# Optimization experiments

Measured on AMD Instinct MI355X. Metric: run time of the kernel, lower is better.

## Reference

```python
import jax, jax.numpy as jnp
import numpy as np

N_SRC = 100000
N_DST = 100000
E = 1600000
D_IN = 128
D_REL = 128
K = 8        # num_heads
D_OUT = 16   # out_dim per head; K*D_OUT = 128
SLOPE = 0.2  # LeakyReLU negative slope


def setup_inputs() -> dict:
    key = jax.random.key(0)
    ks = jax.random.split(key, 11)
    s = 0.05  # weight init scale
    return {
        "feat_src": jax.random.normal(ks[0], (N_SRC, D_IN), jnp.float32),
        "feat_dst": jax.random.normal(ks[1], (N_DST, D_IN), jnp.float32),
        "feat_rel": jax.random.normal(ks[2], (D_REL,), jnp.float32),
        "W_src": jax.random.normal(ks[3], (D_IN, K * D_OUT), jnp.float32) * s,
        "b_src": jnp.zeros((K * D_OUT,), jnp.float32),
        "W_dst": jax.random.normal(ks[4], (D_IN, K * D_OUT), jnp.float32) * s,
        "b_dst": jnp.zeros((K * D_OUT,), jnp.float32),
        "W_rel": jax.random.normal(ks[5], (D_REL, 2 * K * D_OUT), jnp.float32) * s,
        "b_rel": jnp.zeros((2 * K * D_OUT,), jnp.float32),
        "src_idx": jax.random.randint(ks[6], (E,), 0, N_SRC, dtype=jnp.int32),
        "dst_idx": jax.random.randint(ks[7], (E,), 0, N_DST, dtype=jnp.int32),
    }


def reference(feat_src, feat_dst, feat_rel, W_src, b_src, W_dst, b_dst,
              W_rel, b_rel, src_idx, dst_idx):
    # Linear projections (feat_drop = 0 -> identity)
    fs = (feat_src @ W_src + b_src).reshape(-1, K, D_OUT)   # (N_src, K, D)
    fd = (feat_dst @ W_dst + b_dst).reshape(-1, K, D_OUT)   # (N_dst, K, D)
    attn = (feat_rel @ W_rel + b_rel).reshape(K, 2 * D_OUT)  # (K, 2D)

    el = jnp.einsum('nkd,kd->nk', fs, attn[:, :D_OUT])  # (N_src, K)
    er = jnp.einsum('nkd,kd->nk', fd, attn[:, D_OUT:])  # (N_dst, K)

    # Per-edge scores: u_add_v then LeakyReLU
    e = el[src_idx] + er[dst_idx]                        # (E, K)
    e = jnp.where(e >= 0, e, SLOPE * e)

    # edge_softmax: softmax over incoming edges per destination node
    emax = jax.ops.segment_max(e, dst_idx, num_segments=N_DST)  # (N_dst, K)
    a = jnp.exp(e - emax[dst_idx])                               # (E, K)
    asum = jax.ops.segment_sum(a, dst_idx, num_segments=N_DST)   # (N_dst, K)
    a = a / asum[dst_idx]

    # u_mul_e + sum aggregation
    msg = fs[src_idx] * a[:, :, None]                            # (E, K, D)
    out = jax.ops.segment_sum(msg, dst_idx, num_segments=N_DST)  # (N_dst, K, D)
    return out.reshape(N_DST, K * D_OUT)
```

## Files before the change

kernel.cpp:

```cpp
#include <hip/hip_runtime.h>
#include <hip/hip_fp16.h>
#include <hip/hip_bf16.h>

#define SLOPE 0.2f
#define EPB 4096
#define LDA 136
#define CAPLG 12
#define SCAP 1024

typedef short bf16x8 __attribute__((ext_vector_type(8)));
typedef float f32x4 __attribute__((ext_vector_type(4)));

__device__ __forceinline__ unsigned short f2bf(float x) {
    unsigned u = __float_as_uint(x);
    u += 0x7FFFu + ((u >> 16) & 1u);
    return (unsigned short)(u >> 16);
}

__global__ void prep_kernel(const float* __restrict__ feat_rel,
                            const float* __restrict__ W_rel,
                            const float* __restrict__ b_rel,
                            float* __restrict__ attn,
                            const float* __restrict__ W_src,
                            unsigned short* __restrict__ WtS,
                            const float* __restrict__ W_dst,
                            unsigned short* __restrict__ WtD,
                            int* __restrict__ bcur) {
    int bx = blockIdx.x;
    if (bx < 128) {
        const float* W = (bx < 64) ? W_src : W_dst;
        unsigned short* Wt = (bx < 64) ? WtS : WtD;
        int t = (bx & 63) * 256 + threadIdx.x;
        int n = t >> 7, k = t & 127;
        Wt[n * 128 + k] = f2bf(W[k * 128 + n]);
    } else if (bx == 128) {
        int j = threadIdx.x;
        float acc = b_rel[j];
        for (int d = 0; d < 128; ++d)
            acc = fmaf(feat_rel[d], W_rel[d * 256 + j], acc);
        attn[j] = acc;
    } else {
#pragma unroll
        for (int i = 0; i < 4; ++i) {
            int j = threadIdx.x + i * 256;
            bcur[j] = j << CAPLG;
        }
    }
}

#define SMEM_BYTES ((64 * LDA + 128 * LDA) * 2 + 128 * 4)

__global__ __launch_bounds__(256) void gemm_part_kernel(
    const float* __restrict__ featS, const unsigned short* __restrict__ WtS,
    const float* __restrict__ bS,
    const float* __restrict__ featD, const unsigned short* __restrict__ WtD,
    const float* __restrict__ bD,
    const float* __restrict__ attn, __half* __restrict__ fs,
    float* __restrict__ el, float* __restrict__ er,
    int Ms, int Md, int nbs, int ngemm,
    const int* __restrict__ src_idx, const int* __restrict__ dst_idx,
    int* __restrict__ bcur, int* __restrict__ part, int ne)
{
    __shared__ __align__(16) unsigned char smem[SMEM_BYTES];

    int bx = blockIdx.x;
    int t = threadIdx.x;

    if (bx >= ngemm) {
        int* hist = (int*)smem;
        int* base = hist + 1024;
        for (int i = t; i < 1024; i += 256) hist[i] = 0;
        int e0 = (bx - ngemm) * EPB;
        int myS[16], myD[16];
        __syncthreads();
#pragma unroll
        for (int i = 0; i < 16; ++i) {
            int e = e0 + i * 256 + t;
            if (e < ne) {
                myS[i] = src_idx[e];
                myD[i] = dst_idx[e];
                atomicAdd(&hist[myD[i] >> 7], 1);
            } else myD[i] = -1;
        }
        __syncthreads();
        for (int b = t; b < 1024; b += 256) {
            int c = hist[b];
            if (c > 0) {
                base[b] = atomicAdd(&bcur[b], c);
                hist[b] = 0;
            }
        }
        __syncthreads();
#pragma unroll
        for (int i = 0; i < 16; ++i) {
            if (myD[i] >= 0) {
                int b = myD[i] >> 7;
                int slot = base[b] + atomicAdd(&hist[b], 1);
                part[slot] = myS[i] | ((myD[i] & 127) << 20);
            }
        }
        return;
    }

    unsigned short* sA = (unsigned short*)smem;
    unsigned short* sB = sA + 64 * LDA;
    float* sAtt = (float*)(smem + (64 * LDA + 128 * LDA) * 2);

    const float* feat; const unsigned short* Wt; const float* bias;
    __half* f_out; float* e_out; int attn_off, M, row0;
    if (bx < nbs) {
        feat = featS; Wt = WtS; bias = bS; f_out = fs; e_out = el;
        attn_off = 0; M = Ms; row0 = bx * 64;
    } else {
        feat = featD; Wt = WtD; bias = bD; f_out = nullptr; e_out = er;
        attn_off = 16; M = Md; row0 = (bx - nbs) * 64;
    }

    if (t < 128) sAtt[t] = attn[(t >> 4) * 32 + attn_off + (t & 15)];

#pragma unroll
    for (int i = 0; i < 8; ++i) {
        int idx = t + i * 256;
        int row = idx >> 5, k4 = idx & 31;
        int grow = row0 + row;
        float4 v = {0.f, 0.f, 0.f, 0.f};
        if (grow < M) v = *(const float4*)(feat + (size_t)grow * 128 + k4 * 4);
        ushort4 b;
        b.x = f2bf(v.x); b.y = f2bf(v.y); b.z = f2bf(v.z); b.w = f2bf(v.w);
        *(ushort4*)&sA[row * LDA + k4 * 4] = b;
    }
#pragma unroll
    for (int i = 0; i < 8; ++i) {
        int idx = t + i * 256;
        int n = idx >> 4, koff = (idx & 15) * 8;
        *(uint4*)&sB[n * LDA + koff] = *(const uint4*)&Wt[n * 128 + koff];
    }
    __syncthreads();

    int wv = t >> 6, lane = t & 63;
    int m = lane & 15, quad = lane >> 4;
    int n0 = wv * 32;

    f32x4 acc[2][4];
#pragma unroll
    for (int ct = 0; ct < 2; ++ct)
#pragma unroll
        for (int rt = 0; rt < 4; ++rt) acc[ct][rt] = (f32x4){0.f, 0.f, 0.f, 0.f};

#pragma unroll
    for (int ks = 0; ks < 4; ++ks) {
        bf16x8 a[4], b[2];
#pragma unroll
        for (int rt = 0; rt < 4; ++rt)
            a[rt] = *(const bf16x8*)&sA[(rt * 16 + m) * LDA + ks * 32 + quad * 8];
#pragma unroll
        for (int ct = 0; ct < 2; ++ct)
            b[ct] = *(const bf16x8*)&sB[(n0 + ct * 16 + m) * LDA + ks * 32 + quad * 8];
#pragma unroll
        for (int ct = 0; ct < 2; ++ct)
#pragma unroll
            for (int rt = 0; rt < 4; ++rt)
                acc[ct][rt] = __builtin_amdgcn_mfma_f32_16x16x32_bf16(
                    a[rt], b[ct], acc[ct][rt], 0, 0, 0);
    }

    __syncthreads();
    __half* sF = (__half*)sA;
#pragma unroll
    for (int ct = 0; ct < 2; ++ct) {
        int col = n0 + ct * 16 + m;
        float bias_v = bias[col];
#pragma unroll
        for (int rt = 0; rt < 4; ++rt) {
            f32x4 c = acc[ct][rt];
#pragma unroll
            for (int r = 0; r < 4; ++r)
                sF[(rt * 16 + quad * 4 + r) * LDA + col] = __float2half(c[r] + bias_v);
        }
    }
    __syncthreads();

    int mrem = M - row0;

    if (f_out) {
#pragma unroll
        for (int i = 0; i < 4; ++i) {
            int idx = t + i * 256;
            int row = idx >> 4, c8 = (idx & 15) * 8;
            if (row < mrem) {
                uint4 v = *(const uint4*)&sF[row * LDA + c8];
                *(uint4*)(f_out + (size_t)(row0 + row) * 128 + c8) = v;
            }
        }
    }
#pragma unroll
    for (int i = 0; i < 2; ++i) {
        int p = t + i * 256;
        int row = p >> 3, h = p & 7;
        if (row < mrem) {
            const __half* fp = &sF[row * LDA + h * 16];
            const float* ap = &sAtt[h * 16];
            float acc2 = 0.f;
#pragma unroll
            for (int j = 0; j < 16; ++j)
                acc2 = fmaf((float)fp[j], ap[j], acc2);
            e_out[(size_t)(row0 + row) * 8 + h] = acc2;
        }
    }
}

__global__ __launch_bounds__(256) void bucket_agg_kernel(
    const __half* __restrict__ fs, const float* __restrict__ el,
    const float* __restrict__ er, const int* __restrict__ part,
    const int* __restrict__ bcur, float* __restrict__ out,
    int n_dst, int nbuck, int NB8)
{
    __shared__ int csr_l[SCAP];
    __shared__ int cnt[16];
    __shared__ int off16[16];
    __shared__ int cur[16];

    int b = blockIdx.x % NB8;
    int s = blockIdx.x / NB8;
    if (b >= nbuck) return;
    int node0 = (b << 7) + (s << 4);
    if (node0 >= n_dst) return;

    int tid = threadIdx.x;
    if (tid < 16) { cnt[tid] = 0; cur[tid] = 0; }
    int pstart = b << CAPLG;
    int pend = bcur[b];
    __syncthreads();

    for (int pi = pstart + tid; pi < pend; pi += 256) {
        int dl = part[pi] >> 20;
        if ((dl >> 4) == s) atomicAdd(&cnt[dl & 15], 1);
    }
    __syncthreads();
    if (tid == 0) {
        int r = 0;
#pragma unroll
        for (int i = 0; i < 16; ++i) { off16[i] = r; r += cnt[i]; }
    }
    __syncthreads();
    for (int pi = pstart + tid; pi < pend; pi += 256) {
        int val = part[pi];
        int dl = val >> 20;
        if ((dl >> 4) == s) {
            int f = atomicAdd(&cur[dl & 15], 1);
            csr_l[off16[dl & 15] + f] = val & 0xFFFFF;
        }
    }
    __syncthreads();

    int lane = tid & 63;
    int wv = tid >> 6;
    int g = lane >> 4;
    int q = lane & 15;
    int h = q >> 1;
    int nl = wv * 4 + g;
    int node = node0 + nl;
    bool alive = node < n_dst;
    int start = 0, d = 0;
    float er8 = 0.f;
    if (alive) {
        start = off16[nl];
        d = cnt[nl];
        er8 = er[(size_t)node * 8 + h];
    }

    float acc[8] = {0.f, 0.f, 0.f, 0.f, 0.f, 0.f, 0.f, 0.f};
    float wsum = 0.f;
    int i = 0;
    for (; i + 4 <= d; i += 4) {
        int sj[4]; float ex[4]; uint4 v[4];
#pragma unroll
        for (int j = 0; j < 4; ++j)
            sj[j] = csr_l[start + i + j];
#pragma unroll
        for (int j = 0; j < 4; ++j)
            ex[j] = el[(size_t)sj[j] * 8 + h];
#pragma unroll
        for (int j = 0; j < 4; ++j)
            v[j] = *(const uint4*)(fs + (size_t)sj[j] * 128 + q * 8);
#pragma unroll
        for (int j = 0; j < 4; ++j) {
            float x = ex[j] + er8;
            x = (x < 0.f) ? SLOPE * x : x;
            float w = __expf(x);
            const __half* hp = (const __half*)&v[j];
#pragma unroll
            for (int k = 0; k < 8; ++k)
                acc[k] = fmaf(w, (float)hp[k], acc[k]);
            wsum += w;
        }
    }
    for (; i < d; ++i) {
        int s0 = csr_l[start + i];
        float x = el[(size_t)s0 * 8 + h] + er8;
        x = (x < 0.f) ? SLOPE * x : x;
        float w0 = __expf(x);
        uint4 v0 = *(const uint4*)(fs + (size_t)s0 * 128 + q * 8);
        const __half* hp = (const __half*)&v0;
#pragma unroll
        for (int k = 0; k < 8; ++k)
            acc[k] = fmaf(w0, (float)hp[k], acc[k]);
        wsum += w0;
    }
    if (alive) {
        float inv = (d > 0) ? 1.0f / wsum : 0.f;
        f32x4 o0 = {acc[0] * inv, acc[1] * inv, acc[2] * inv, acc[3] * inv};
        f32x4 o1 = {acc[4] * inv, acc[5] * inv, acc[6] * inv, acc[7] * inv};
        __builtin_nontemporal_store(o0, (f32x4*)(out + (size_t)node * 128 + q * 8));
        __builtin_nontemporal_store(o1, (f32x4*)(out + (size_t)node * 128 + q * 8 + 4));
    }
}

extern "C" void kernel_launch(void* const* d_in, const int* in_sizes, int n_in,
                              void* d_out, int out_size, void* d_ws, size_t ws_size,
                              hipStream_t stream) {
    const float* feat_src = (const float*)d_in[0];
    const float* feat_dst = (const float*)d_in[1];
    const float* feat_rel = (const float*)d_in[2];
    const float* W_src    = (const float*)d_in[3];
    const float* b_src    = (const float*)d_in[4];
    const float* W_dst    = (const float*)d_in[5];
    const float* b_dst    = (const float*)d_in[6];
    const float* W_rel    = (const float*)d_in[7];
    const float* b_rel    = (const float*)d_in[8];
    const int*   src_idx  = (const int*)d_in[9];
    const int*   dst_idx  = (const int*)d_in[10];
    float* out = (float*)d_out;

    int n_src = in_sizes[0] / 128;
    int n_dst = in_sizes[1] / 128;
    int ne    = in_sizes[9];
    int nbuck = (n_dst + 127) >> 7;
    int NB8   = (nbuck + 7) & ~7;
    size_t slab = (size_t)nbuck << CAPLG;

    char* w = (char*)d_ws;
    auto alloc = [&](size_t b) { char* p = w; w += (b + 255) & ~(size_t)255; return p; };
    __half* fs   = (__half*)alloc((size_t)n_src * 128 * 2);
    float*  el   = (float*)alloc((size_t)n_src * 8 * 4);
    float*  er   = (float*)alloc((size_t)n_dst * 8 * 4);
    float*  attn = (float*)alloc(256 * 4);
    unsigned short* WtS = (unsigned short*)alloc(128 * 128 * 2);
    unsigned short* WtD = (unsigned short*)alloc(128 * 128 * 2);
    int*    bcur = (int*)alloc(1024 * 4);
    int*    part = (int*)alloc(slab * 4);

    prep_kernel<<<130, 256, 0, stream>>>(
        feat_rel, W_rel, b_rel, attn, W_src, WtS, W_dst, WtD, bcur);

    int nbs = (n_src + 63) / 64, nbd = (n_dst + 63) / 64;
    int ngemm = nbs + nbd;
    int nparts = (ne + EPB - 1) / EPB;
    gemm_part_kernel<<<ngemm + nparts, 256, 0, stream>>>(
        feat_src, WtS, b_src, feat_dst, WtD, b_dst, attn,
        fs, el, er, n_src, n_dst, nbs, ngemm,
        src_idx, dst_idx, bcur, part, ne);

    bucket_agg_kernel<<<NB8 * 8, 256, 0, stream>>>(
        fs, el, er, part, bcur, out, n_dst, nbuck, NB8);
}
```

Baseline: 283.4 us.

## Fuse prep into GEMM blocks and drop counting pass in bucket aggregation

Removes the separate prep kernel. Each GEMM block now computes the attention vector from W_rel and transposes and converts the fp32 weights to bf16 itself, and a memset initialises the bucket counters. The bucket aggregation kernel drops its first counting pass over the partition list and scatters source indices into fixed 64-entry per-node slots. This saves one launch and one pass over the partition data. In exchange, every GEMM block repeats the attention and weight-transpose work with strided loads, and any node with more than 64 incoming edges silently loses edges.

```diff
diff --git a/kernel.cpp b/kernel.cpp
--- a/kernel.cpp
+++ b/kernel.cpp
@@ -6,7 +6,7 @@
 #define EPB 4096
 #define LDA 136
 #define CAPLG 12
-#define SCAP 1024
+#define NCAP 64
 
 typedef short bf16x8 __attribute__((ext_vector_type(8)));
 typedef float f32x4 __attribute__((ext_vector_type(4)));
@@ -17,46 +17,16 @@
     return (unsigned short)(u >> 16);
 }
 
-__global__ void prep_kernel(const float* __restrict__ feat_rel,
-                            const float* __restrict__ W_rel,
-                            const float* __restrict__ b_rel,
-                            float* __restrict__ attn,
-                            const float* __restrict__ W_src,
-                            unsigned short* __restrict__ WtS,
-                            const float* __restrict__ W_dst,
-                            unsigned short* __restrict__ WtD,
-                            int* __restrict__ bcur) {
-    int bx = blockIdx.x;
-    if (bx < 128) {
-        const float* W = (bx < 64) ? W_src : W_dst;
-        unsigned short* Wt = (bx < 64) ? WtS : WtD;
-        int t = (bx & 63) * 256 + threadIdx.x;
-        int n = t >> 7, k = t & 127;
-        Wt[n * 128 + k] = f2bf(W[k * 128 + n]);
-    } else if (bx == 128) {
-        int j = threadIdx.x;
-        float acc = b_rel[j];
-        for (int d = 0; d < 128; ++d)
-            acc = fmaf(feat_rel[d], W_rel[d * 256 + j], acc);
-        attn[j] = acc;
-    } else {
-#pragma unroll
-        for (int i = 0; i < 4; ++i) {
-            int j = threadIdx.x + i * 256;
-            bcur[j] = j << CAPLG;
-        }
-    }
-}
-
 #define SMEM_BYTES ((64 * LDA + 128 * LDA) * 2 + 128 * 4)
 
 __global__ __launch_bounds__(256) void gemm_part_kernel(
-    const float* __restrict__ featS, const unsigned short* __restrict__ WtS,
+    const float* __restrict__ featS, const float* __restrict__ WS,
     const float* __restrict__ bS,
-    const float* __restrict__ featD, const unsigned short* __restrict__ WtD,
+    const float* __restrict__ featD, const float* __restrict__ WD,
     const float* __restrict__ bD,
-    const float* __restrict__ attn, __half* __restrict__ fs,
-    float* __restrict__ el, float* __restrict__ er,
+    const float* __restrict__ feat_rel, const float* __restrict__ W_rel,
+    const float* __restrict__ b_rel,
+    __half* __restrict__ fs, float* __restrict__ el, float* __restrict__ er,
     int Ms, int Md, int nbs, int ngemm,
     const int* __restrict__ src_idx, const int* __restrict__ dst_idx,
     int* __restrict__ bcur, int* __restrict__ part, int ne)
@@ -86,7 +56,7 @@
         for (int b = t; b < 1024; b += 256) {
             int c = hist[b];
             if (c > 0) {
-                base[b] = atomicAdd(&bcur[b], c);
+                base[b] = (b << CAPLG) + atomicAdd(&bcur[b], c);
                 hist[b] = 0;
             }
         }
@@ -106,17 +76,23 @@
     unsigned short* sB = sA + 64 * LDA;
     float* sAtt = (float*)(smem + (64 * LDA + 128 * LDA) * 2);
 
-    const float* feat; const unsigned short* Wt; const float* bias;
+    const float* feat; const float* W; const float* bias;
     __half* f_out; float* e_out; int attn_off, M, row0;
     if (bx < nbs) {
-        feat = featS; Wt = WtS; bias = bS; f_out = fs; e_out = el;
+        feat = featS; W = WS; bias = bS; f_out = fs; e_out = el;
         attn_off = 0; M = Ms; row0 = bx * 64;
     } else {
-        feat = featD; Wt = WtD; bias = bD; f_out = nullptr; e_out = er;
+        feat = featD; W = WD; bias = bD; f_out = nullptr; e_out = er;
         attn_off = 16; M = Md; row0 = (bx - nbs) * 64;
     }
 
-    if (t < 128) sAtt[t] = attn[(t >> 4) * 32 + attn_off + (t & 15)];
+    if (t < 128) {
+        int j = (t >> 4) * 32 + attn_off + (t & 15);
+        float a = b_rel[j];
+        for (int d = 0; d < 128; ++d)
+            a = fmaf(feat_rel[d], W_rel[d * 256 + j], a);
+        sAtt[t] = a;
+    }
 
 #pragma unroll
     for (int i = 0; i < 8; ++i) {
@@ -132,8 +108,12 @@
 #pragma unroll
     for (int i = 0; i < 8; ++i) {
         int idx = t + i * 256;
-        int n = idx >> 4, koff = (idx & 15) * 8;
-        *(uint4*)&sB[n * LDA + koff] = *(const uint4*)&Wt[n * 128 + koff];
+        int n = idx & 127, kc = (idx >> 7) * 8;
+        unsigned short tmp[8];
+#pragma unroll
+        for (int j = 0; j < 8; ++j)
+            tmp[j] = f2bf(W[(size_t)(kc + j) * 128 + n]);
+        *(uint4*)&sB[n * LDA + kc] = *(uint4*)tmp;
     }
     __syncthreads();
 
@@ -215,9 +195,7 @@
     const int* __restrict__ bcur, float* __restrict__ out,
     int n_dst, int nbuck, int NB8)
 {
-    __shared__ int csr_l[SCAP];
-    __shared__ int cnt[16];
-    __shared__ int off16[16];
+    __shared__ int csr_l[16 * NCAP];
     __shared__ int cur[16];
 
     int b = blockIdx.x % NB8;
@@ -227,28 +205,17 @@
     if (node0 >= n_dst) return;
 
     int tid = threadIdx.x;
-    if (tid < 16) { cnt[tid] = 0; cur[tid] = 0; }
+    if (tid < 16) cur[tid] = 0;
     int pstart = b << CAPLG;
-    int pend = bcur[b];
-    __syncthreads();
-
-    for (int pi = pstart + tid; pi < pend; pi += 256) {
-        int dl = part[pi] >> 20;
-        if ((dl >> 4) == s) atomicAdd(&cnt[dl & 15], 1);
-    }
-    __syncthreads();
-    if (tid == 0) {
-        int r = 0;
-#pragma unroll
-        for (int i = 0; i < 16; ++i) { off16[i] = r; r += cnt[i]; }
-    }
-    __syncthreads();
+    int pend = pstart + bcur[b];
+    __syncthreads();
+
     for (int pi = pstart + tid; pi < pend; pi += 256) {
         int val = part[pi];
         int dl = val >> 20;
         if ((dl >> 4) == s) {
             int f = atomicAdd(&cur[dl & 15], 1);
-            csr_l[off16[dl & 15] + f] = val & 0xFFFFF;
+            if (f < NCAP) csr_l[(dl & 15) * NCAP + f] = val & 0xFFFFF;
         }
     }
     __syncthreads();
@@ -261,11 +228,11 @@
     int nl = wv * 4 + g;
     int node = node0 + nl;
     bool alive = node < n_dst;
-    int start = 0, d = 0;
+    int start = nl * NCAP;
+    int d = 0;
     float er8 = 0.f;
     if (alive) {
-        start = off16[nl];
-        d = cnt[nl];
+        d = cur[nl]; if (d > NCAP) d = NCAP;
         er8 = er[(size_t)node * 8 + h];
     }
 
@@ -344,20 +311,17 @@
     __half* fs   = (__half*)alloc((size_t)n_src * 128 * 2);
     float*  el   = (float*)alloc((size_t)n_src * 8 * 4);
     float*  er   = (float*)alloc((size_t)n_dst * 8 * 4);
-    float*  attn = (float*)alloc(256 * 4);
-    unsigned short* WtS = (unsigned short*)alloc(128 * 128 * 2);
-    unsigned short* WtD = (unsigned short*)alloc(128 * 128 * 2);
     int*    bcur = (int*)alloc(1024 * 4);
     int*    part = (int*)alloc(slab * 4);
 
-    prep_kernel<<<130, 256, 0, stream>>>(
-        feat_rel, W_rel, b_rel, attn, W_src, WtS, W_dst, WtD, bcur);
+    (void)hipMemsetAsync(bcur, 0, 1024 * 4, stream);
 
     int nbs = (n_src + 63) / 64, nbd = (n_dst + 63) / 64;
     int ngemm = nbs + nbd;
     int nparts = (ne + EPB - 1) / EPB;
     gemm_part_kernel<<<ngemm + nparts, 256, 0, stream>>>(
-        feat_src, WtS, b_src, feat_dst, WtD, b_dst, attn,
+        feat_src, W_src, b_src, feat_dst, W_dst, b_dst,
+        feat_rel, W_rel, b_rel,
         fs, el, er, n_src, n_dst, nbs, ngemm,
         src_idx, dst_idx, bcur, part, ne);
 
```

New measurement: 304.5 us. 1.07x slower.
